# Performance work log

Measured on AMD Instinct MI355X. Metric: run time of the kernel, lower is better.

The kernel has to match this reference:

```python
import jax, jax.numpy as jnp
import numpy as np

SMOOTH = 9.0   # self.labmda
EPS = 1e-8
MASK_VAL = -1.0

I, R, D = 64, 36, 1024   # n_image, n_regions, d
C, W = 64, 32            # n_caption, max_n_word


def setup_inputs() -> dict:
    key = jax.random.key(0)
    k1, k2, k3, k4 = jax.random.split(key, 4)
    imgs = jax.random.normal(k1, (I, R, D), dtype=jnp.float32)
    caps = jax.random.normal(k2, (C, W, D), dtype=jnp.float32)
    img_lens = jax.random.randint(k3, (I,), 1, R + 1)
    cap_lens = jnp.maximum(jax.random.randint(k4, (C,), 0, W + 1), 4)
    return {"imgs": imgs, "caps": caps, "img_lens": img_lens, "cap_lens": cap_lens}


def reference(imgs, caps, img_lens, cap_lens):
    # imgs: (I,R,D) images/regions; caps: (C,W,D); cap_lens: (C,)
    # Vectorized over captions: padded word positions are masked so the
    # per-caption word-dim l2norm matches the ragged torch loop exactly.
    wmask = jnp.arange(W)[None, :] < cap_lens[:, None]          # (C,W)
    wmask_f = wmask.astype(imgs.dtype)

    # attn[c,i,w,r] = <caps[c,w], imgs[i,r]>  (torch: bmm(context, queryT))
    attn = jnp.einsum('ird,cwd->ciwr', imgs, caps)              # (C,I,W,R)
    attn = jax.nn.leaky_relu(attn, 0.1)
    attn = attn * wmask_f[:, None, :, None]                     # zero padded words
    # l2norm over word dim (torch l2norm(attn, 2) on (I,R,W)): eps after sqrt
    norm_w = jnp.sqrt(jnp.sum(attn * attn, axis=2, keepdims=True)) + EPS
    attn = attn / norm_w
    # temperature-scaled softmax over regions
    attn = jax.nn.softmax(attn * SMOOTH, axis=3)                # (C,I,W,R)

    # weighted context per word, l2-normalized over feature dim
    wctx = jnp.einsum('ciwr,ird->ciwd', attn, imgs)             # (C,I,W,D)
    wctx = wctx / (jnp.sqrt(jnp.sum(wctx * wctx, axis=-1, keepdims=True)) + EPS)

    # cosine similarity between the word and its attended context
    cap_e = caps[:, None, :, :]                                 # (C,1,W,D)
    w12 = jnp.sum(cap_e * wctx, axis=-1)                        # (C,I,W)
    w1 = jnp.sqrt(jnp.sum(cap_e * cap_e, axis=-1))
    w2 = jnp.sqrt(jnp.sum(wctx * wctx, axis=-1))
    sim = w12 / jnp.maximum(w1 * w2, EPS)                       # (C,I,W)

    sim = jnp.where(wmask[:, None, :], sim, MASK_VAL)
    return jnp.transpose(sim, (1, 0, 2))                        # (I,C,W)
```

## Files before the change

kernel.cpp:

```cpp
#include <hip/hip_runtime.h>
#include <hip/hip_bf16.h>

#define IDIM 64
#define RDIM 36
#define DDIM 1024
#define CDIM 64
#define WDIM 32
#define SMOOTH 9.0f
#define EPSF 1e-8f

typedef __bf16 bf16_t;
typedef __bf16 bf16x8 __attribute__((ext_vector_type(8)));
typedef __bf16 bf16x4 __attribute__((ext_vector_type(4)));
typedef float f32x4 __attribute__((ext_vector_type(4)));

#define MFMA16(a, b, c) __builtin_amdgcn_mfma_f32_16x16x32_bf16((a), (b), (c), 0, 0, 0)

#define IMGSB_OFF 0
#define IMGSB_BYTES (IDIM * 4 * 8 * 3 * 512 * 2)
#define CAPSA_OFF (IMGSB_OFF + IMGSB_BYTES)
#define CAPSA_BYTES (CDIM * 4 * 8 * 2 * 512 * 2)
#define GF_OFF    (CAPSA_OFF + CAPSA_BYTES)
#define GF_BYTES  (IDIM * 384 * 8 * 2)
#define CAPN_OFF  (GF_OFF + GF_BYTES)

__global__ __launch_bounds__(256) void prep_kernel(
    const float* __restrict__ imgs, const float* __restrict__ caps,
    bf16_t* __restrict__ imgsB, bf16_t* __restrict__ capsA) {
  __shared__ __align__(16) bf16_t ldsb[36 * 264];
  int b = blockIdx.x, tid = threadIdx.x;
  if (b < 256) {
    int i = b >> 2, wvk = b & 3, ks = wvk * 256;
    const float* src = imgs + (size_t)i * RDIM * DDIM + ks;
#pragma unroll
    for (int rep = 0; rep < 9; ++rep) {
      int idx = rep * 256 + tid;
      int row = idx >> 6, q = idx & 63;
      float4 v = *(const float4*)(src + (size_t)row * DDIM + q * 4);
      bf16x4 p;
      p[0] = (bf16_t)v.x; p[1] = (bf16_t)v.y; p[2] = (bf16_t)v.z; p[3] = (bf16_t)v.w;
      *(bf16x4*)&ldsb[row * 264 + q * 4] = p;
    }
    __syncthreads();
    bf16_t* dst = imgsB + (size_t)(i * 4 + wvk) * 12288;
#pragma unroll
    for (int rep = 0; rep < 6; ++rep) {
      int u = rep * 256 + tid;
      int kk = u / 192, rem = u - kk * 192;
      int nt = rem >> 6, lane = rem & 63, qd = lane >> 4, l15 = lane & 15;
      int row = nt * 16 + l15;
      bf16x8 p;
      if (row < 36) {
        p = *(const bf16x8*)&ldsb[row * 264 + kk * 32 + qd * 8];
      } else {
#pragma unroll
        for (int j = 0; j < 8; ++j) p[j] = (bf16_t)0.0f;
      }
      *(bf16x8*)(dst + (size_t)u * 8) = p;
    }
  } else {
    int bb = b - 256;
    int c = bb >> 2, wvk = bb & 3, ks = wvk * 256;
    const float* src = caps + (size_t)c * WDIM * DDIM + ks;
#pragma unroll
    for (int rep = 0; rep < 8; ++rep) {
      int idx = rep * 256 + tid;
      int row = idx >> 6, q = idx & 63;
      float4 v = *(const float4*)(src + (size_t)row * DDIM + q * 4);
      bf16x4 p;
      p[0] = (bf16_t)v.x; p[1] = (bf16_t)v.y; p[2] = (bf16_t)v.z; p[3] = (bf16_t)v.w;
      *(bf16x4*)&ldsb[row * 264 + q * 4] = p;
    }
    __syncthreads();
    bf16_t* dst = capsA + (size_t)(c * 4 + wvk) * 8192;
#pragma unroll
    for (int rep = 0; rep < 4; ++rep) {
      int u = rep * 256 + tid;
      int kk = u >> 7, rem = u & 127;
      int mt = rem >> 6, lane = rem & 63, qd = lane >> 4, l15 = lane & 15;
      int row = mt * 16 + l15;
      bf16x8 p = *(const bf16x8*)&ldsb[row * 264 + kk * 32 + qd * 8];
      *(bf16x8*)(dst + (size_t)u * 8) = p;
    }
  }
}

__global__ __launch_bounds__(256) void gram_kernel(
    const bf16_t* __restrict__ imgsB, const bf16_t* __restrict__ capsA,
    bf16_t* __restrict__ Gfrag, float* __restrict__ capnorm) {
  __shared__ float part[4][48][49];
  __shared__ float cnl[4][32];
  int bx = blockIdx.x;
  int tid = threadIdx.x, wv = tid >> 6, ln = tid & 63;
  int l15 = ln & 15, qd = ln >> 4;
  if (bx < 64) {
    int i = bx;
    const bf16_t* base = imgsB + (size_t)(i * 4 + wv) * 12288;
    f32x4 acc[3][3];
#pragma unroll
    for (int mt = 0; mt < 3; ++mt)
#pragma unroll
      for (int nt = 0; nt < 3; ++nt) {
        f32x4 zf = {0.f, 0.f, 0.f, 0.f};
        acc[mt][nt] = zf;
      }
#pragma unroll
    for (int kk = 0; kk < 8; ++kk) {
      bf16x8 a[3];
#pragma unroll
      for (int nt = 0; nt < 3; ++nt)
        a[nt] = *(const bf16x8*)(base + ((size_t)(kk * 3 + nt) * 64 + ln) * 8);
#pragma unroll
      for (int mt = 0; mt < 3; ++mt)
#pragma unroll
        for (int nt = 0; nt < 3; ++nt)
          acc[mt][nt] = MFMA16(a[mt], a[nt], acc[mt][nt]);
    }
#pragma unroll
    for (int mt = 0; mt < 3; ++mt)
#pragma unroll
      for (int nt = 0; nt < 3; ++nt)
#pragma unroll
        for (int rg = 0; rg < 4; ++rg)
          part[wv][mt * 16 + qd * 4 + rg][nt * 16 + l15] = acc[mt][nt][rg];
    __syncthreads();
    for (int idx = tid; idx < 384; idx += 256) {
      int kk = idx / 192;
      int rem = idx - kk * 192;
      int nt = rem >> 6, lnn = rem & 63;
      int qd2 = lnn >> 4, l152 = lnn & 15;
      int n = nt * 16 + l152;
      bf16x8 pk;
#pragma unroll
      for (int j = 0; j < 8; ++j) {
        int k = kk * 32 + qd2 * 8 + j;
        float v = (k < 48) ? (part[0][k][n] + part[1][k][n] + part[2][k][n] + part[3][k][n]) : 0.f;
        pk[j] = (bf16_t)v;
      }
      *(bf16x8*)(Gfrag + ((size_t)i * 384 + idx) * 8) = pk;
    }
  } else {
    int c = bx - 64;
    const bf16_t* base = capsA + (size_t)(c * 4 + wv) * 8192;
    float ss0 = 0.f, ss1 = 0.f;
#pragma unroll
    for (int kk = 0; kk < 8; ++kk) {
      bf16x8 p0 = *(const bf16x8*)(base + ((size_t)(kk * 2 + 0) * 64 + ln) * 8);
      bf16x8 p1 = *(const bf16x8*)(base + ((size_t)(kk * 2 + 1) * 64 + ln) * 8);
#pragma unroll
      for (int j = 0; j < 8; ++j) {
        float v0 = (float)p0[j], v1 = (float)p1[j];
        ss0 += v0 * v0;
        ss1 += v1 * v1;
      }
    }
    ss0 += __shfl_xor(ss0, 16, 64); ss0 += __shfl_xor(ss0, 32, 64);
    ss1 += __shfl_xor(ss1, 16, 64); ss1 += __shfl_xor(ss1, 32, 64);
    if (qd == 0) { cnl[wv][l15] = ss0; cnl[wv][16 + l15] = ss1; }
    __syncthreads();
    if (tid < 32)
      capnorm[c * 32 + tid] = sqrtf(cnl[0][tid] + cnl[1][tid] + cnl[2][tid] + cnl[3][tid]);
  }
}

__global__ __launch_bounds__(256, 2) void main_kernel(
    const bf16_t* __restrict__ capsA, const bf16_t* __restrict__ imgsB,
    const bf16_t* __restrict__ Gfrag, const float* __restrict__ capnorm,
    const int* __restrict__ cap_lens, float* __restrict__ out) {
  __shared__ __align__(16) bf16_t attnS[8][2304];

  int bx = blockIdx.x;
  int wv = threadIdx.x >> 6, ln = threadIdx.x & 63;
  int l15 = ln & 15, qd = ln >> 4;
  int xcd = bx & 7, rest = bx >> 3;
  int ig = xcd * 2 + (rest & 1);
  int cpair = rest >> 1;
  int i = ig * 4 + wv;
  int c0 = cpair * 2;
  int clen[2] = {cap_lens[c0], cap_lens[c0 + 1]};

  const bf16_t* Ab = capsA + (size_t)c0 * 32768;
  const bf16_t* Bb = imgsB + (size_t)i * 49152;

  f32x4 acc[2][2][3];
#pragma unroll
  for (int t = 0; t < 2; ++t)
#pragma unroll
    for (int mt = 0; mt < 2; ++mt)
#pragma unroll
      for (int nt = 0; nt < 3; ++nt) {
        f32x4 zf = {0.f, 0.f, 0.f, 0.f};
        acc[t][mt][nt] = zf;
      }
#pragma unroll 4
  for (int s = 0; s < 32; ++s) {
    const bf16_t* ap = Ab + (size_t)s * 1024 + ln * 8;
    const bf16_t* bp = Bb + (size_t)s * 1536 + ln * 8;
    bf16x8 a00 = *(const bf16x8*)(ap);
    bf16x8 a01 = *(const bf16x8*)(ap + 512);
    bf16x8 a10 = *(const bf16x8*)(ap + 32768);
    bf16x8 a11 = *(const bf16x8*)(ap + 33280);
    bf16x8 b0 = *(const bf16x8*)(bp);
    bf16x8 b1 = *(const bf16x8*)(bp + 512);
    bf16x8 b2 = *(const bf16x8*)(bp + 1024);
    acc[0][0][0] = MFMA16(a00, b0, acc[0][0][0]);
    acc[0][0][1] = MFMA16(a00, b1, acc[0][0][1]);
    acc[0][0][2] = MFMA16(a00, b2, acc[0][0][2]);
    acc[0][1][0] = MFMA16(a01, b0, acc[0][1][0]);
    acc[0][1][1] = MFMA16(a01, b1, acc[0][1][1]);
    acc[0][1][2] = MFMA16(a01, b2, acc[0][1][2]);
    acc[1][0][0] = MFMA16(a10, b0, acc[1][0][0]);
    acc[1][0][1] = MFMA16(a10, b1, acc[1][0][1]);
    acc[1][0][2] = MFMA16(a10, b2, acc[1][0][2]);
    acc[1][1][0] = MFMA16(a11, b0, acc[1][1][0]);
    acc[1][1][1] = MFMA16(a11, b1, acc[1][1][1]);
    acc[1][1][2] = MFMA16(a11, b2, acc[1][1][2]);
  }

  const bf16_t* Gb = Gfrag + (size_t)i * 3072;
  bf16x8 ga[2][3];
#pragma unroll
  for (int kk = 0; kk < 2; ++kk)
#pragma unroll
    for (int nt = 0; nt < 3; ++nt)
      ga[kk][nt] = *(const bf16x8*)(Gb + ((size_t)(kk * 3 + nt) * 64 + ln) * 8);

  float attnv[2][2][3][4];
  float Srow[2][2][4];
  float n2row[2][2][4];

#pragma unroll
  for (int t = 0; t < 2; ++t) {
#pragma unroll
    for (int mt = 0; mt < 2; ++mt)
#pragma unroll
      for (int nt = 0; nt < 3; ++nt) {
        bool padn = (nt == 2) && (l15 >= 4);
#pragma unroll
        for (int rg = 0; rg < 4; ++rg) {
          float v = acc[t][mt][nt][rg];
          float l = (v > 0.f) ? v : 0.1f * v;
          int m = mt * 16 + qd * 4 + rg;
          if (m >= clen[t] || padn) l = 0.f;
          attnv[t][mt][nt][rg] = l;
        }
      }
    float sinv[3];
#pragma unroll
    for (int nt = 0; nt < 3; ++nt) {
      float ns = 0.f;
#pragma unroll
      for (int mt = 0; mt < 2; ++mt)
#pragma unroll
        for (int rg = 0; rg < 4; ++rg) {
          float t2 = attnv[t][mt][nt][rg];
          ns += t2 * t2;
        }
      ns += __shfl_xor(ns, 16, 64);
      ns += __shfl_xor(ns, 32, 64);
      sinv[nt] = SMOOTH / (sqrtf(ns) + EPSF);
    }
#pragma unroll
    for (int mt = 0; mt < 2; ++mt)
#pragma unroll
      for (int rg = 0; rg < 4; ++rg) {
        float z[3];
#pragma unroll
        for (int nt = 0; nt < 3; ++nt) {
          float v = attnv[t][mt][nt][rg] * sinv[nt];
          if (nt == 2 && l15 >= 4) v = -1e30f;
          z[nt] = v;
        }
        float mx = fmaxf(fmaxf(z[0], z[1]), z[2]);
#pragma unroll
        for (int off = 1; off < 16; off <<= 1) mx = fmaxf(mx, __shfl_xor(mx, off, 64));
        float e[3], es = 0.f;
#pragma unroll
        for (int nt = 0; nt < 3; ++nt) {
          e[nt] = __expf(z[nt] - mx);
          es += e[nt];
        }
#pragma unroll
        for (int off = 1; off < 16; off <<= 1) es += __shfl_xor(es, off, 64);
        float inv = 1.0f / es;
        float sac = 0.f;
#pragma unroll
        for (int nt = 0; nt < 3; ++nt) {
          float a = e[nt] * inv;
          attnv[t][mt][nt][rg] = a;
          sac += a * acc[t][mt][nt][rg];
        }
#pragma unroll
        for (int off = 1; off < 16; off <<= 1) sac += __shfl_xor(sac, off, 64);
        Srow[t][mt][rg] = sac;
      }
    bf16_t* as = &attnS[wv * 2 + t][0];
#pragma unroll
    for (int mt = 0; mt < 2; ++mt)
#pragma unroll
      for (int nt = 0; nt < 3; ++nt)
#pragma unroll
        for (int rg = 0; rg < 4; ++rg)
          as[(mt * 16 + qd * 4 + rg) * 72 + nt * 16 + l15] = (bf16_t)attnv[t][mt][nt][rg];
    {
      bf16x8 z8;
#pragma unroll
      for (int q = 0; q < 8; ++q) z8[q] = (bf16_t)0.0f;
      *(bf16x8*)(as + (ln >> 1) * 72 + 48 + (ln & 1) * 8) = z8;
    }
    bf16x8 fa[2][2];
#pragma unroll
    for (int mt = 0; mt < 2; ++mt)
#pragma unroll
      for (int kk = 0; kk < 2; ++kk)
        fa[mt][kk] = *(const bf16x8*)(as + (mt * 16 + l15) * 72 + kk * 32 + qd * 8);
    f32x4 y[2][3];
#pragma unroll
    for (int mt = 0; mt < 2; ++mt)
#pragma unroll
      for (int nt = 0; nt < 3; ++nt) {
        f32x4 zf = {0.f, 0.f, 0.f, 0.f};
        y[mt][nt] = zf;
      }
#pragma unroll
    for (int kk = 0; kk < 2; ++kk)
#pragma unroll
      for (int mt = 0; mt < 2; ++mt)
#pragma unroll
        for (int nt = 0; nt < 3; ++nt)
          y[mt][nt] = MFMA16(fa[mt][kk], ga[kk][nt], y[mt][nt]);
#pragma unroll
    for (int mt = 0; mt < 2; ++mt)
#pragma unroll
      for (int rg = 0; rg < 4; ++rg) {
        float nn = 0.f;
#pragma unroll
        for (int nt = 0; nt < 3; ++nt) nn += y[mt][nt][rg] * attnv[t][mt][nt][rg];
#pragma unroll
        for (int off = 1; off < 16; off <<= 1) nn += __shfl_xor(nn, off, 64);
        n2row[t][mt][rg] = nn;
      }
  }

#pragma unroll
  for (int t = 0; t < 2; ++t) {
    if (l15 < 2) {
      int mt = l15;
      int c = c0 + t;
      f32x4 cn = *(const f32x4*)(capnorm + c * 32 + mt * 16 + qd * 4);
      f32x4 o;
#pragma unroll
      for (int rg = 0; rg < 4; ++rg) {
        float n2v = fmaxf(n2row[t][mt][rg], 0.f);
        float nrm = sqrtf(n2v);
        float den = nrm + EPSF;
        float w12 = Srow[t][mt][rg] / den;
        float w2 = nrm / den;
        float sim = w12 / fmaxf(cn[rg] * w2, EPSF);
        int m = mt * 16 + qd * 4 + rg;
        if (m >= clen[t]) sim = -1.0f;
        o[rg] = sim;
      }
      *(f32x4*)(out + ((size_t)i * CDIM + c) * WDIM + mt * 16 + qd * 4) = o;
    }
  }
}

extern "C" void kernel_launch(void* const* d_in, const int* in_sizes, int n_in,
                              void* d_out, int out_size, void* d_ws, size_t ws_size,
                              hipStream_t stream) {
  const float* imgs = (const float*)d_in[0];
  const float* caps = (const float*)d_in[1];
  const int* cap_lens = (const int*)d_in[3];
  float* out = (float*)d_out;

  char* ws = (char*)d_ws;
  bf16_t* imgsB = (bf16_t*)(ws + IMGSB_OFF);
  bf16_t* capsA = (bf16_t*)(ws + CAPSA_OFF);
  bf16_t* Gfrag = (bf16_t*)(ws + GF_OFF);
  float* capnorm = (float*)(ws + CAPN_OFF);

  prep_kernel<<<512, 256, 0, stream>>>(imgs, caps, imgsB, capsA);
  gram_kernel<<<128, 256, 0, stream>>>(imgsB, capsA, Gfrag, capnorm);
  main_kernel<<<512, 256, 0, stream>>>(capsA, imgsB, Gfrag, capnorm, cap_lens, out);
}
```

Measured before the change: 117.5 us.

## Process one caption per wave to halve registers and double grid occupancy

Each block now handles a single caption against four images instead of two captions, so the grid grows from 512 to 1024 blocks. Launch bounds rise to 4 waves per SIMD and the shared attention buffer halves. The leaky-relu values are recomputed from the accumulators rather than stored, which cuts register pressure. The trade-off is that the image fragments are no longer reused across two captions, so global loads of imgsB double.

```diff
diff --git a/kernel.cpp b/kernel.cpp
--- a/kernel.cpp
+++ b/kernel.cpp
@@ -163,58 +163,46 @@
   }
 }
 
-__global__ __launch_bounds__(256, 2) void main_kernel(
+__global__ __launch_bounds__(256, 4) void main_kernel(
     const bf16_t* __restrict__ capsA, const bf16_t* __restrict__ imgsB,
     const bf16_t* __restrict__ Gfrag, const float* __restrict__ capnorm,
     const int* __restrict__ cap_lens, float* __restrict__ out) {
-  __shared__ __align__(16) bf16_t attnS[8][2304];
+  __shared__ __align__(16) bf16_t attnS[4][32 * 72];
 
   int bx = blockIdx.x;
   int wv = threadIdx.x >> 6, ln = threadIdx.x & 63;
   int l15 = ln & 15, qd = ln >> 4;
-  int xcd = bx & 7, rest = bx >> 3;
-  int ig = xcd * 2 + (rest & 1);
-  int cpair = rest >> 1;
-  int i = ig * 4 + wv;
-  int c0 = cpair * 2;
-  int clen[2] = {cap_lens[c0], cap_lens[c0 + 1]};
-
-  const bf16_t* Ab = capsA + (size_t)c0 * 32768;
-  const bf16_t* Bb = imgsB + (size_t)i * 49152;
-
-  f32x4 acc[2][2][3];
-#pragma unroll
-  for (int t = 0; t < 2; ++t)
-#pragma unroll
-    for (int mt = 0; mt < 2; ++mt)
-#pragma unroll
-      for (int nt = 0; nt < 3; ++nt) {
-        f32x4 zf = {0.f, 0.f, 0.f, 0.f};
-        acc[t][mt][nt] = zf;
-      }
+  int xcd = bx & 7, t = bx >> 3;
+  int c = t & 63, ih = t >> 6;
+  int i = xcd * 8 + ih * 4 + wv;
+  int clen = cap_lens[c];
+
+  const bf16_t* Ab = capsA + (size_t)c * (4 * 8 * 2 * 512);
+  const bf16_t* Bb = imgsB + (size_t)i * (4 * 8 * 3 * 512);
+
+  f32x4 acc[2][3];
+#pragma unroll
+  for (int mt = 0; mt < 2; ++mt)
+#pragma unroll
+    for (int nt = 0; nt < 3; ++nt) {
+      f32x4 zf = {0.f, 0.f, 0.f, 0.f};
+      acc[mt][nt] = zf;
+    }
 #pragma unroll 4
   for (int s = 0; s < 32; ++s) {
     const bf16_t* ap = Ab + (size_t)s * 1024 + ln * 8;
     const bf16_t* bp = Bb + (size_t)s * 1536 + ln * 8;
-    bf16x8 a00 = *(const bf16x8*)(ap);
-    bf16x8 a01 = *(const bf16x8*)(ap + 512);
-    bf16x8 a10 = *(const bf16x8*)(ap + 32768);
-    bf16x8 a11 = *(const bf16x8*)(ap + 33280);
+    bf16x8 a0 = *(const bf16x8*)(ap);
+    bf16x8 a1 = *(const bf16x8*)(ap + 512);
     bf16x8 b0 = *(const bf16x8*)(bp);
     bf16x8 b1 = *(const bf16x8*)(bp + 512);
     bf16x8 b2 = *(const bf16x8*)(bp + 1024);
-    acc[0][0][0] = MFMA16(a00, b0, acc[0][0][0]);
-    acc[0][0][1] = MFMA16(a00, b1, acc[0][0][1]);
-    acc[0][0][2] = MFMA16(a00, b2, acc[0][0][2]);
-    acc[0][1][0] = MFMA16(a01, b0, acc[0][1][0]);
-    acc[0][1][1] = MFMA16(a01, b1, acc[0][1][1]);
-    acc[0][1][2] = MFMA16(a01, b2, acc[0][1][2]);
-    acc[1][0][0] = MFMA16(a10, b0, acc[1][0][0]);
-    acc[1][0][1] = MFMA16(a10, b1, acc[1][0][1]);
-    acc[1][0][2] = MFMA16(a10, b2, acc[1][0][2]);
-    acc[1][1][0] = MFMA16(a11, b0, acc[1][1][0]);
-    acc[1][1][1] = MFMA16(a11, b1, acc[1][1][1]);
-    acc[1][1][2] = MFMA16(a11, b2, acc[1][1][2]);
+    acc[0][0] = MFMA16(a0, b0, acc[0][0]);
+    acc[0][1] = MFMA16(a0, b1, acc[0][1]);
+    acc[0][2] = MFMA16(a0, b2, acc[0][2]);
+    acc[1][0] = MFMA16(a1, b0, acc[1][0]);
+    acc[1][1] = MFMA16(a1, b1, acc[1][1]);
+    acc[1][2] = MFMA16(a1, b2, acc[1][2]);
   }
 
   const bf16_t* Gb = Gfrag + (size_t)i * 3072;
@@ -225,144 +213,134 @@
     for (int nt = 0; nt < 3; ++nt)
       ga[kk][nt] = *(const bf16x8*)(Gb + ((size_t)(kk * 3 + nt) * 64 + ln) * 8);
 
-  float attnv[2][2][3][4];
-  float Srow[2][2][4];
-  float n2row[2][2][4];
-
-#pragma unroll
-  for (int t = 0; t < 2; ++t) {
+  float sinv[3];
+#pragma unroll
+  for (int nt = 0; nt < 3; ++nt) {
+    bool padn = (nt == 2) && (l15 >= 4);
+    float ns = 0.f;
 #pragma unroll
     for (int mt = 0; mt < 2; ++mt)
 #pragma unroll
+      for (int rg = 0; rg < 4; ++rg) {
+        float v = acc[mt][nt][rg];
+        float l = (v > 0.f) ? v : 0.1f * v;
+        int m = mt * 16 + qd * 4 + rg;
+        if (m >= clen || padn) l = 0.f;
+        ns += l * l;
+      }
+    ns += __shfl_xor(ns, 16, 64);
+    ns += __shfl_xor(ns, 32, 64);
+    sinv[nt] = SMOOTH / (sqrtf(ns) + EPSF);
+  }
+
+  float Srow[2][4];
+#pragma unroll
+  for (int mt = 0; mt < 2; ++mt)
+#pragma unroll
+    for (int rg = 0; rg < 4; ++rg) {
+      int m = mt * 16 + qd * 4 + rg;
+      bool mrow = (m >= clen);
+      float z[3];
+#pragma unroll
       for (int nt = 0; nt < 3; ++nt) {
-        bool padn = (nt == 2) && (l15 >= 4);
-#pragma unroll
-        for (int rg = 0; rg < 4; ++rg) {
-          float v = acc[t][mt][nt][rg];
-          float l = (v > 0.f) ? v : 0.1f * v;
-          int m = mt * 16 + qd * 4 + rg;
-          if (m >= clen[t] || padn) l = 0.f;
-          attnv[t][mt][nt][rg] = l;
-        }
-      }
-    float sinv[3];
+        float v = acc[mt][nt][rg];
+        float l = (v > 0.f) ? v : 0.1f * v;
+        if (mrow) l = 0.f;
+        float zz = l * sinv[nt];
+        if (nt == 2 && l15 >= 4) zz = -1e30f;
+        z[nt] = zz;
+      }
+      float mx = fmaxf(fmaxf(z[0], z[1]), z[2]);
+#pragma unroll
+      for (int off = 1; off < 16; off <<= 1) mx = fmaxf(mx, __shfl_xor(mx, off, 64));
+      float e[3], es = 0.f;
+#pragma unroll
+      for (int nt = 0; nt < 3; ++nt) {
+        e[nt] = __expf(z[nt] - mx);
+        es += e[nt];
+      }
+#pragma unroll
+      for (int off = 1; off < 16; off <<= 1) es += __shfl_xor(es, off, 64);
+      float inv = 1.0f / es;
+      float sac = 0.f;
+#pragma unroll
+      for (int nt = 0; nt < 3; ++nt) {
+        float a = e[nt] * inv;
+        sac += a * acc[mt][nt][rg];
+        acc[mt][nt][rg] = a;
+      }
+#pragma unroll
+      for (int off = 1; off < 16; off <<= 1) sac += __shfl_xor(sac, off, 64);
+      Srow[mt][rg] = sac;
+    }
+
+  bf16_t* as = &attnS[wv][0];
+#pragma unroll
+  for (int mt = 0; mt < 2; ++mt)
+#pragma unroll
+    for (int nt = 0; nt < 3; ++nt)
+#pragma unroll
+      for (int rg = 0; rg < 4; ++rg)
+        as[(mt * 16 + qd * 4 + rg) * 72 + nt * 16 + l15] = (bf16_t)acc[mt][nt][rg];
+  {
+    bf16x8 z8;
+#pragma unroll
+    for (int q = 0; q < 8; ++q) z8[q] = (bf16_t)0.0f;
+    *(bf16x8*)(as + (ln >> 1) * 72 + 48 + (ln & 1) * 8) = z8;
+  }
+  bf16x8 fa[2][2];
+#pragma unroll
+  for (int mt = 0; mt < 2; ++mt)
+#pragma unroll
+    for (int kk = 0; kk < 2; ++kk)
+      fa[mt][kk] = *(const bf16x8*)(as + (mt * 16 + l15) * 72 + kk * 32 + qd * 8);
+
+  f32x4 y[2][3];
+#pragma unroll
+  for (int mt = 0; mt < 2; ++mt)
 #pragma unroll
     for (int nt = 0; nt < 3; ++nt) {
-      float ns = 0.f;
-#pragma unroll
-      for (int mt = 0; mt < 2; ++mt)
-#pragma unroll
-        for (int rg = 0; rg < 4; ++rg) {
-          float t2 = attnv[t][mt][nt][rg];
-          ns += t2 * t2;
-        }
-      ns += __shfl_xor(ns, 16, 64);
-      ns += __shfl_xor(ns, 32, 64);
-      sinv[nt] = SMOOTH / (sqrtf(ns) + EPSF);
-    }
+      f32x4 zf = {0.f, 0.f, 0.f, 0.f};
+      y[mt][nt] = zf;
+    }
+#pragma unroll
+  for (int kk = 0; kk < 2; ++kk)
 #pragma unroll
     for (int mt = 0; mt < 2; ++mt)
 #pragma unroll
-      for (int rg = 0; rg < 4; ++rg) {
-        float z[3];
-#pragma unroll
-        for (int nt = 0; nt < 3; ++nt) {
-          float v = attnv[t][mt][nt][rg] * sinv[nt];
-          if (nt == 2 && l15 >= 4) v = -1e30f;
-          z[nt] = v;
-        }
-        float mx = fmaxf(fmaxf(z[0], z[1]), z[2]);
-#pragma unroll
-        for (int off = 1; off < 16; off <<= 1) mx = fmaxf(mx, __shfl_xor(mx, off, 64));
-        float e[3], es = 0.f;
-#pragma unroll
-        for (int nt = 0; nt < 3; ++nt) {
-          e[nt] = __expf(z[nt] - mx);
-          es += e[nt];
-        }
-#pragma unroll
-        for (int off = 1; off < 16; off <<= 1) es += __shfl_xor(es, off, 64);
-        float inv = 1.0f / es;
-        float sac = 0.f;
-#pragma unroll
-        for (int nt = 0; nt < 3; ++nt) {
-          float a = e[nt] * inv;
-          attnv[t][mt][nt][rg] = a;
-          sac += a * acc[t][mt][nt][rg];
-        }
-#pragma unroll
-        for (int off = 1; off < 16; off <<= 1) sac += __shfl_xor(sac, off, 64);
-        Srow[t][mt][rg] = sac;
-      }
-    bf16_t* as = &attnS[wv * 2 + t][0];
-#pragma unroll
-    for (int mt = 0; mt < 2; ++mt)
-#pragma unroll
       for (int nt = 0; nt < 3; ++nt)
-#pragma unroll
-        for (int rg = 0; rg < 4; ++rg)
-          as[(mt * 16 + qd * 4 + rg) * 72 + nt * 16 + l15] = (bf16_t)attnv[t][mt][nt][rg];
-    {
-      bf16x8 z8;
-#pragma unroll
-      for (int q = 0; q < 8; ++q) z8[q] = (bf16_t)0.0f;
-      *(bf16x8*)(as + (ln >> 1) * 72 + 48 + (ln & 1) * 8) = z8;
-    }
-    bf16x8 fa[2][2];
-#pragma unroll
-    for (int mt = 0; mt < 2; ++mt)
-#pragma unroll
-      for (int kk = 0; kk < 2; ++kk)
-        fa[mt][kk] = *(const bf16x8*)(as + (mt * 16 + l15) * 72 + kk * 32 + qd * 8);
-    f32x4 y[2][3];
-#pragma unroll
-    for (int mt = 0; mt < 2; ++mt)
-#pragma unroll
-      for (int nt = 0; nt < 3; ++nt) {
-        f32x4 zf = {0.f, 0.f, 0.f, 0.f};
-        y[mt][nt] = zf;
-      }
-#pragma unroll
-    for (int kk = 0; kk < 2; ++kk)
-#pragma unroll
-      for (int mt = 0; mt < 2; ++mt)
-#pragma unroll
-        for (int nt = 0; nt < 3; ++nt)
-          y[mt][nt] = MFMA16(fa[mt][kk], ga[kk][nt], y[mt][nt]);
-#pragma unroll
-    for (int mt = 0; mt < 2; ++mt)
-#pragma unroll
-      for (int rg = 0; rg < 4; ++rg) {
-        float nn = 0.f;
-#pragma unroll
-        for (int nt = 0; nt < 3; ++nt) nn += y[mt][nt][rg] * attnv[t][mt][nt][rg];
-#pragma unroll
-        for (int off = 1; off < 16; off <<= 1) nn += __shfl_xor(nn, off, 64);
-        n2row[t][mt][rg] = nn;
-      }
-  }
-
-#pragma unroll
-  for (int t = 0; t < 2; ++t) {
-    if (l15 < 2) {
-      int mt = l15;
-      int c = c0 + t;
-      f32x4 cn = *(const f32x4*)(capnorm + c * 32 + mt * 16 + qd * 4);
-      f32x4 o;
-#pragma unroll
-      for (int rg = 0; rg < 4; ++rg) {
-        float n2v = fmaxf(n2row[t][mt][rg], 0.f);
-        float nrm = sqrtf(n2v);
-        float den = nrm + EPSF;
-        float w12 = Srow[t][mt][rg] / den;
-        float w2 = nrm / den;
-        float sim = w12 / fmaxf(cn[rg] * w2, EPSF);
-        int m = mt * 16 + qd * 4 + rg;
-        if (m >= clen[t]) sim = -1.0f;
-        o[rg] = sim;
-      }
-      *(f32x4*)(out + ((size_t)i * CDIM + c) * WDIM + mt * 16 + qd * 4) = o;
-    }
+        y[mt][nt] = MFMA16(fa[mt][kk], ga[kk][nt], y[mt][nt]);
+
+  float n2row[2][4];
+#pragma unroll
+  for (int mt = 0; mt < 2; ++mt)
+#pragma unroll
+    for (int rg = 0; rg < 4; ++rg) {
+      float nn = 0.f;
+#pragma unroll
+      for (int nt = 0; nt < 3; ++nt) nn += y[mt][nt][rg] * acc[mt][nt][rg];
+#pragma unroll
+      for (int off = 1; off < 16; off <<= 1) nn += __shfl_xor(nn, off, 64);
+      n2row[mt][rg] = nn;
+    }
+
+  if (l15 < 2) {
+    int mt = l15;
+    f32x4 cn = *(const f32x4*)(capnorm + c * 32 + mt * 16 + qd * 4);
+    f32x4 o;
+#pragma unroll
+    for (int rg = 0; rg < 4; ++rg) {
+      float n2v = fmaxf(n2row[mt][rg], 0.f);
+      float nrm = sqrtf(n2v);
+      float den = nrm + EPSF;
+      float w12 = Srow[mt][rg] / den;
+      float w2 = nrm / den;
+      float sim = w12 / fmaxf(cn[rg] * w2, EPSF);
+      int m = mt * 16 + qd * 4 + rg;
+      if (m >= clen) sim = -1.0f;
+      o[rg] = sim;
+    }
+    *(f32x4*)(out + ((size_t)i * CDIM + c) * WDIM + mt * 16 + qd * 4) = o;
   }
 }
 
@@ -382,5 +360,5 @@
 
   prep_kernel<<<512, 256, 0, stream>>>(imgs, caps, imgsB, capsA);
   gram_kernel<<<128, 256, 0, stream>>>(imgsB, capsA, Gfrag, capnorm);
-  main_kernel<<<512, 256, 0, stream>>>(capsA, imgsB, Gfrag, capnorm, cap_lens, out);
+  main_kernel<<<1024, 256, 0, stream>>>(capsA, imgsB, Gfrag, capnorm, cap_lens, out);
 }
```

After: 106.1 us. -9.7%, faster.
